# Kernel optimization log

Hardware: AMD Instinct MI355X
Metric: run time of the kernel (lower is better)

The kernel has to match this reference:

```python
import jax, jax.numpy as jnp
import numpy as np

NUM_HEADS = 4
WINDOW_LIST = ((8, 8), (16, 16))
SHIFT_LIST = ((0, 0), (8, 8))


def _window_attn(s, window, shift, num_heads):
    # s: (b, c, h, w) with c = 2 * num_heads * head_dim
    b, c, h, w = s.shape
    ws1, ws2 = window
    # reflect-pad bottom/right to a multiple of the window size
    ph = (-h) % ws1
    pw = (-w) % ws2
    if ph or pw:
        s = jnp.pad(s, ((0, 0), (0, 0), (0, ph), (0, pw)), mode='reflect')
    if shift != (0, 0):
        s = jnp.roll(s, shift, axis=(2, 3))
    H, W = s.shape[2], s.shape[3]
    nh, nw = H // ws1, W // ws2
    ch = c // (2 * num_heads)
    # b (qv head ch) (nh ws1) (nw ws2) -> qv b head nh nw (ws1 ws2) ch
    t = s.reshape(b, 2, num_heads, ch, nh, ws1, nw, ws2)
    t = t.transpose(1, 0, 2, 4, 6, 5, 7, 3)
    t = t.reshape(2, b, num_heads, nh, nw, ws1 * ws2, ch)
    q, v = t[0], t[1]
    # per-window self-attention: scores = q @ q^T (no scaling, as in source)
    attn = jax.nn.softmax(jnp.einsum('bhnwtc,bhnwsc->bhnwts', q, q), axis=-1)
    out = jnp.einsum('bhnwts,bhnwsc->bhnwtc', attn, v)
    # merge windows back: -> b (head ch) (nh ws1) (nw ws2)
    out = out.reshape(b, num_heads, nh, nw, ws1, ws2, ch)
    out = out.transpose(0, 1, 6, 2, 4, 3, 5).reshape(b, num_heads * ch, nh * ws1, nw * ws2)
    if shift != (0, 0):
        out = jnp.roll(out, (-shift[0], -shift[1]), axis=(2, 3))
    return out[:, :, :h, :w]


def setup_inputs() -> dict:
    key = jax.random.key(0)
    x = jax.random.normal(key, (4, 64, 256, 256), dtype=jnp.float32)
    return {"x": x}


def reference(x):
    n = len(WINDOW_LIST)
    cs = x.shape[1] // n
    outs = [
        _window_attn(x[:, i * cs:(i + 1) * cs], win, sh, NUM_HEADS)
        for i, (win, sh) in enumerate(zip(WINDOW_LIST, SHIFT_LIST))
    ]
    # attn_layer / proj_layer are Identity by default
    return jnp.concatenate(outs, axis=1)
```

## Files before the change

kernel.cpp:

```cpp
#include <hip/hip_runtime.h>
#include <math.h>


typedef __attribute__((ext_vector_type(4))) float f32x4;
typedef __attribute__((ext_vector_type(8))) short short8;
typedef __attribute__((ext_vector_type(4))) unsigned short ushort4v;

static constexpr int Ww = 256;
static constexpr int CIN = 64;
static constexpr int COUT = 32;
static constexpr size_t PLANE = 65536;
static constexpr float ALPHA = 1.2011224087864498f;

__device__ inline float fexp2(float x) {
#if __has_builtin(__builtin_amdgcn_exp2f)
    return __builtin_amdgcn_exp2f(x);
#else
    float r;
    asm("v_exp_f32 %0, %1" : "=v"(r) : "v"(x));
    return r;
#endif
}

__device__ inline unsigned cvt_pk_bf16(float lo, float hi) {
    unsigned r;
    asm("v_cvt_pk_bf16_f32 %0, %1, %2" : "=v"(r) : "v"(lo), "v"(hi));
    return r;
}

__device__ inline unsigned short bfhi_u(float x) {
    union { float f; unsigned u; } u; u.f = x;
    return (unsigned short)(u.u >> 16);
}
__device__ inline float bf2f(unsigned short h) {
    union { unsigned u; float f; } u; u.u = ((unsigned)h) << 16;
    return u.f;
}
__device__ inline unsigned short bf_rne(float x) {
    union { float f; unsigned u; } u; u.f = x;
    return (unsigned short)((u.u + 0x7FFFu + ((u.u >> 16) & 1u)) >> 16);
}

struct Smem16 {
    unsigned short qpack[4][256][8];
    unsigned short vh[4][4][260];
    float l_lds[4][256];
};
struct Smem8 {
    float4 qs[8][64];
    float4 vs[8][64];
};
union SmemU { Smem16 a; Smem8 b; };

__global__ __launch_bounds__(512) void fused_attn(const float* __restrict__ x,
                                                  float* __restrict__ out) {
    __shared__ __align__(16) SmemU smem;

    const int tid  = threadIdx.x;
    const int lane = tid & 63;
    const int wave = tid >> 6;

    if (blockIdx.x < 1024) {
        const int blk = blockIdx.x;
        const int wj = blk & 15, wi = (blk >> 4) & 15, b = blk >> 8;
        const int head = wave >> 1;
        const int half = wave & 1;
        const int g = lane >> 4;
        const int n = lane & 15;

#pragma unroll
        for (int k = 0; k < 16; ++k) {
            const int f = k * 512 + tid;
            const int c = f >> 8;
            const int t = f & 255;
            const int gi = (wi * 16 + (t >> 4) + 248) & 255;
            const int gj = (wj * 16 + (t & 15) + 248) & 255;
            float val = x[((size_t)b * CIN + 32 + c) * PLANE + (size_t)gi * Ww + gj];
            const int h = (c >> 2) & 3, ch = c & 3;
            if (c < 16) {
                val *= ALPHA;
                const unsigned short hi = bfhi_u(val);
                smem.a.qpack[h][t][ch]     = hi;
                smem.a.qpack[h][t][4 + ch] = bfhi_u(val - bf2f(hi));
            } else {
                smem.a.vh[h][ch][t] = bf_rne(val);
            }
        }
        __syncthreads();

        const int tbase = half * 128;

        const unsigned long long m0  = (g == 0) ? ~0ull : 0ull;
        const unsigned long long m1  = (g == 1) ? ~0ull : 0ull;
        const unsigned long long m01 = (g <  2) ? ~0ull : 0ull;

        short8 BQ[8];
#pragma unroll
        for (int m = 0; m < 8; ++m) {
            union { short8 v; unsigned long long q[2]; } u, f;
            u.v = *(const short8*)&smem.a.qpack[head][tbase + m * 16 + n][0];
            f.q[0] = (u.q[0] & m0) | (u.q[1] & m1);
            f.q[1] = u.q[0] & m0;
            BQ[m] = f.v;
        }

        f32x4 O[8];
#pragma unroll
        for (int m = 0; m < 8; ++m) O[m] = (f32x4){0.f, 0.f, 0.f, 0.f};
        const f32x4 zero4 = (f32x4){0.f, 0.f, 0.f, 0.f};

        for (int c = 0; c < 8; ++c) {
            short8 AQ[2];
#pragma unroll
            for (int a = 0; a < 2; ++a) {
                union { short8 v; unsigned long long q[2]; } u, f;
                u.v = *(const short8*)&smem.a.qpack[head][c * 32 + a * 16 + n][0];
                f.q[0] = u.q[0] & m01;
                f.q[1] = u.q[1] & m0;
                AQ[a] = f.v;
            }

            short8 Vhf = {0, 0, 0, 0, 0, 0, 0, 0};
            if (n < 4) {
                const int s0 = c * 32 + 4 * g;
                const ushort4v va = *(const ushort4v*)&smem.a.vh[head][n][s0];
                const ushort4v vb = *(const ushort4v*)&smem.a.vh[head][n][s0 + 16];
#pragma unroll
                for (int j = 0; j < 4; ++j) { Vhf[j] = (short)va[j]; Vhf[4 + j] = (short)vb[j]; }
            } else if (n == 4) {
#pragma unroll
                for (int j = 0; j < 8; ++j) Vhf[j] = (short)0x3F80;
            }

#pragma unroll
            for (int m = 0; m < 8; ++m) {
                const f32x4 c0 = __builtin_amdgcn_mfma_f32_16x16x32_bf16(AQ[0], BQ[m], zero4, 0, 0, 0);
                const f32x4 c1 = __builtin_amdgcn_mfma_f32_16x16x32_bf16(AQ[1], BQ[m], zero4, 0, 0, 0);
                union { unsigned u[4]; short8 s; } pk;
                pk.u[0] = cvt_pk_bf16(fexp2(c0[0]), fexp2(c0[1]));
                pk.u[1] = cvt_pk_bf16(fexp2(c0[2]), fexp2(c0[3]));
                pk.u[2] = cvt_pk_bf16(fexp2(c1[0]), fexp2(c1[1]));
                pk.u[3] = cvt_pk_bf16(fexp2(c1[2]), fexp2(c1[3]));
                O[m] = __builtin_amdgcn_mfma_f32_16x16x32_bf16(pk.s, Vhf, O[m], 0, 0, 0);
            }
        }

        if (n == 4) {
#pragma unroll
            for (int m = 0; m < 8; ++m)
#pragma unroll
                for (int r = 0; r < 4; ++r)
                    smem.a.l_lds[head][tbase + m * 16 + 4 * g + r] = __builtin_amdgcn_rcpf(O[m][r]);
        }
        if (n < 4) {
            float* op = out + ((size_t)b * COUT + 16 + head * 4 + n) * PLANE;
#pragma unroll
            for (int m = 0; m < 8; ++m) {
                const f32x4 inv4 = *(const f32x4*)&smem.a.l_lds[head][tbase + m * 16 + 4 * g];
                const int gi  = (wi * 16 + half * 8 + m + 248) & 255;
                const int gj0 = (wj * 16 + 4 * g + 248) & 255;
                f32x4 res;
                res[0] = O[m][0] * inv4[0];
                res[1] = O[m][1] * inv4[1];
                res[2] = O[m][2] * inv4[2];
                res[3] = O[m][3] * inv4[3];
                *(f32x4*)(op + (size_t)gi * Ww + gj0) = res;
            }
        }
    } else {
        int bid = (blockIdx.x - 1024) * 8 + wave;
        const int wj   = bid & 31; bid >>= 5;
        const int wi   = bid & 31; bid >>= 5;
        const int head = bid & 3;  bid >>= 2;
        const int b    = bid;

        const int t  = lane;
        const int gi = wi * 8 + (t >> 3);
        const int gj = wj * 8 + (t & 7);
        const size_t pix = (size_t)gi * Ww + gj;

        const float* xq = x + (size_t)b * CIN * PLANE + (size_t)(head * 4) * PLANE + pix;
        const float* xv = xq + 16 * PLANE;

        float4* qs = smem.b.qs[wave];
        float4* vs = smem.b.vs[wave];

        float4 q, v;
        q.x = xq[0] * ALPHA; q.y = xq[PLANE] * ALPHA;
        q.z = xq[2 * PLANE] * ALPHA; q.w = xq[3 * PLANE] * ALPHA;
        v.x = xv[0];         v.y = xv[PLANE];     v.z = xv[2 * PLANE]; v.w = xv[3 * PLANE];
        qs[t] = q;
        vs[t] = v;

        float l = 0.f;
        float4 acc = make_float4(0.f, 0.f, 0.f, 0.f);
#pragma unroll
        for (int s = 0; s < 64; ++s) {
            const float4 p = qs[s];
            const float d = q.x * p.x + q.y * p.y + q.z * p.z + q.w * p.w;
            const float e = fexp2(d);
            l += e;
            const float4 vv = vs[s];
            acc.x += e * vv.x; acc.y += e * vv.y;
            acc.z += e * vv.z; acc.w += e * vv.w;
        }
        const float inv = 1.0f / l;

        float* ob = out + (size_t)b * COUT * PLANE + (size_t)(head * 4) * PLANE + pix;
        ob[0]         = acc.x * inv;
        ob[PLANE]     = acc.y * inv;
        ob[2 * PLANE] = acc.z * inv;
        ob[3 * PLANE] = acc.w * inv;
    }
}

extern "C" void kernel_launch(void* const* d_in, const int* in_sizes, int n_in,
                              void* d_out, int out_size, void* d_ws, size_t ws_size,
                              hipStream_t stream) {
    const float* x = (const float*)d_in[0];
    float* out = (float*)d_out;

    hipLaunchKernelGGL(fused_attn, dim3(3072), dim3(512), 0, stream, x, out);
}
```

Measured before the change: 59.53 us.

## Interleave block types, pre-permute V in LDS, use packed f32 math

Block scheduling now interleaves the 16x16-window blocks with the 8x8-window blocks (one of every three blocks) instead of running all heavy blocks first, to balance load across the grid. V is stored in LDS pre-permuted, with a ones row for the row sums, so each lane loads its MFMA B operand with a single 16-byte read instead of gathering and branching. The 8x8 path uses v_pk_mul/v_pk_fma packed FP32 ops for the dot products and accumulation. The gains depend on scheduling and instruction-issue effects, and the inline asm may limit what the compiler can optimize.

```diff
diff --git a/kernel.cpp b/kernel.cpp
--- a/kernel.cpp
+++ b/kernel.cpp
@@ -3,8 +3,8 @@
 
 
 typedef __attribute__((ext_vector_type(4))) float f32x4;
+typedef __attribute__((ext_vector_type(2))) float f32x2;
 typedef __attribute__((ext_vector_type(8))) short short8;
-typedef __attribute__((ext_vector_type(4))) unsigned short ushort4v;
 
 static constexpr int Ww = 256;
 static constexpr int CIN = 64;
@@ -28,6 +28,17 @@
     return r;
 }
 
+__device__ inline f32x2 pk_mul(f32x2 a, f32x2 b) {
+    f32x2 r;
+    asm("v_pk_mul_f32 %0, %1, %2" : "=v"(r) : "v"(a), "v"(b));
+    return r;
+}
+__device__ inline f32x2 pk_fma(f32x2 a, f32x2 b, f32x2 c) {
+    f32x2 r;
+    asm("v_pk_fma_f32 %0, %1, %2, %3" : "=v"(r) : "v"(a), "v"(b), "v"(c));
+    return r;
+}
+
 __device__ inline unsigned short bfhi_u(float x) {
     union { float f; unsigned u; } u; u.f = x;
     return (unsigned short)(u.u >> 16);
@@ -43,7 +54,7 @@
 
 struct Smem16 {
     unsigned short qpack[4][256][8];
-    unsigned short vh[4][4][260];
+    unsigned short vperm[4][5][272];
     float l_lds[4][256];
 };
 struct Smem8 {
@@ -59,9 +70,12 @@
     const int tid  = threadIdx.x;
     const int lane = tid & 63;
     const int wave = tid >> 6;
-
-    if (blockIdx.x < 1024) {
-        const int blk = blockIdx.x;
+    const int bid  = blockIdx.x;
+    const int q3   = bid / 3;
+    const int r3   = bid - q3 * 3;
+
+    if (r3 == 0) {
+        const int blk = q3;
         const int wj = blk & 15, wi = (blk >> 4) & 15, b = blk >> 8;
         const int head = wave >> 1;
         const int half = wave & 1;
@@ -83,8 +97,15 @@
                 smem.a.qpack[h][t][ch]     = hi;
                 smem.a.qpack[h][t][4 + ch] = bfhi_u(val - bf2f(hi));
             } else {
-                smem.a.vh[h][ch][t] = bf_rne(val);
-            }
+                const int rr = t & 31;
+                const int pos = (t & ~31) + ((rr >> 2) & 3) * 8 + (rr >> 4) * 4 + (rr & 3);
+                smem.a.vperm[h][ch][pos] = bf_rne(val);
+            }
+        }
+#pragma unroll
+        for (int k = 0; k < 2; ++k) {
+            const int i = k * 512 + tid;
+            smem.a.vperm[i >> 8][4][i & 255] = (unsigned short)0x3F80;
         }
         __syncthreads();
 
@@ -121,16 +142,7 @@
             }
 
             short8 Vhf = {0, 0, 0, 0, 0, 0, 0, 0};
-            if (n < 4) {
-                const int s0 = c * 32 + 4 * g;
-                const ushort4v va = *(const ushort4v*)&smem.a.vh[head][n][s0];
-                const ushort4v vb = *(const ushort4v*)&smem.a.vh[head][n][s0 + 16];
-#pragma unroll
-                for (int j = 0; j < 4; ++j) { Vhf[j] = (short)va[j]; Vhf[4 + j] = (short)vb[j]; }
-            } else if (n == 4) {
-#pragma unroll
-                for (int j = 0; j < 8; ++j) Vhf[j] = (short)0x3F80;
-            }
+            if (n < 5) Vhf = *(const short8*)&smem.a.vperm[head][n][c * 32 + g * 8];
 
 #pragma unroll
             for (int m = 0; m < 8; ++m) {
@@ -168,11 +180,11 @@
             }
         }
     } else {
-        int bid = (blockIdx.x - 1024) * 8 + wave;
-        const int wj   = bid & 31; bid >>= 5;
-        const int wi   = bid & 31; bid >>= 5;
-        const int head = bid & 3;  bid >>= 2;
-        const int b    = bid;
+        int bid8 = (q3 * 2 + r3 - 1) * 8 + wave;
+        const int wj   = bid8 & 31; bid8 >>= 5;
+        const int wi   = bid8 & 31; bid8 >>= 5;
+        const int head = bid8 & 3;  bid8 >>= 2;
+        const int b    = bid8;
 
         const int t  = lane;
         const int gi = wi * 8 + (t >> 3);
@@ -192,25 +204,28 @@
         qs[t] = q;
         vs[t] = v;
 
+        const f32x2 qxy = {q.x, q.y}, qzw = {q.z, q.w};
         float l = 0.f;
-        float4 acc = make_float4(0.f, 0.f, 0.f, 0.f);
+        f32x2 acc01 = {0.f, 0.f}, acc23 = {0.f, 0.f};
 #pragma unroll
         for (int s = 0; s < 64; ++s) {
             const float4 p = qs[s];
-            const float d = q.x * p.x + q.y * p.y + q.z * p.z + q.w * p.w;
-            const float e = fexp2(d);
+            f32x2 d2 = pk_mul(qxy, (f32x2){p.x, p.y});
+            d2 = pk_fma(qzw, (f32x2){p.z, p.w}, d2);
+            const float e = fexp2(d2[0] + d2[1]);
             l += e;
+            const f32x2 e2 = {e, e};
             const float4 vv = vs[s];
-            acc.x += e * vv.x; acc.y += e * vv.y;
-            acc.z += e * vv.z; acc.w += e * vv.w;
+            acc01 = pk_fma(e2, (f32x2){vv.x, vv.y}, acc01);
+            acc23 = pk_fma(e2, (f32x2){vv.z, vv.w}, acc23);
         }
         const float inv = 1.0f / l;
 
         float* ob = out + (size_t)b * COUT * PLANE + (size_t)(head * 4) * PLANE + pix;
-        ob[0]         = acc.x * inv;
-        ob[PLANE]     = acc.y * inv;
-        ob[2 * PLANE] = acc.z * inv;
-        ob[3 * PLANE] = acc.w * inv;
+        ob[0]         = acc01[0] * inv;
+        ob[PLANE]     = acc01[1] * inv;
+        ob[2 * PLANE] = acc23[0] * inv;
+        ob[3 * PLANE] = acc23[1] * inv;
     }
 }
 
```

New measurement: 67.56 us. +13.5%, slower.
